# Kernel optimization log

Hardware: AMD Instinct MI355X
Metric: run time of the kernel (lower is better)

The kernel has to match this reference:

```python
import jax, jax.numpy as jnp
import numpy as np

B, N, M, D, H, K, V = 2, 2048, 2048, 1024, 16, 64, 64
MAX_WAVELENGTH = 10000
SCALE_FACTOR = 1.0


def rope(x, positions, max_wavelength, scale_factor):
    # x: [b, s, h, k]; positions: [b, s] int
    head_dim = x.shape[-1]
    fraction = 2.0 * jnp.arange(head_dim // 2, dtype=x.dtype) / head_dim
    timescale = jnp.asarray(max_wavelength, x.dtype) ** fraction            # [k/2]
    # scaled positions -> phase per (b, s, 1 head bcast, k/2)
    phase = (positions.astype(x.dtype) / scale_factor)[:, :, None, None] / timescale  # [b,s,1,k/2]
    sin, cos = jnp.sin(phase), jnp.cos(phase)
    x1, x2 = jnp.split(x, 2, axis=-1)
    return jnp.concatenate([x1 * cos - x2 * sin, x2 * cos + x1 * sin], axis=-1)


def setup_inputs() -> dict:
    key = jax.random.key(0)
    ks = jax.random.split(key, 8)
    scale = 1.0 / np.sqrt(D)  # keep logits numerically sane with random params
    inp = {
        "query": jax.random.normal(ks[0], (B, N, D), jnp.float32),
        "q_positions": jnp.broadcast_to(jnp.arange(N, dtype=jnp.int32), (B, N)),
        "key": jax.random.normal(ks[1], (B, M, D), jnp.float32),
        "k_positions": jnp.broadcast_to(jnp.arange(M, dtype=jnp.int32), (B, M)),
        "value": jax.random.normal(ks[2], (B, M, D), jnp.float32),
        "mask": jnp.ones((1, 1, N, M), dtype=bool),
        "P_q": jax.random.normal(ks[3], (H, D, K), jnp.float32) * scale,
        "P_k": jax.random.normal(ks[4], (H, D, K), jnp.float32) * scale,
        "P_v": jax.random.normal(ks[5], (H, D, V), jnp.float32) * scale,
        "P_o": jax.random.normal(ks[6], (H, D, V), jnp.float32) * scale,
    }
    return inp


def reference(query, q_positions, key, k_positions, value, mask, P_q, P_k, P_v, P_o):
    q = jnp.einsum('bnd,hdk->bnhk', query, P_q)
    k = jnp.einsum('bmd,hdk->bmhk', key, P_k)
    v = jnp.einsum('bmd,hdv->bmhv', value, P_v)
    q = rope(q, q_positions, MAX_WAVELENGTH, SCALE_FACTOR)
    k = rope(k, k_positions, MAX_WAVELENGTH, SCALE_FACTOR)
    logits = jnp.einsum('bnhk,bmhk->bhnm', q, k)
    if mask is not None:
        logits = jnp.where(mask, logits, -jnp.inf)
    weights = jax.nn.softmax(logits, axis=-1)
    o = jnp.einsum('bhnm,bmhv->bnhv', weights, v)
    return jnp.einsum('bnhv,hdv->bnd', o, P_o)
```

## Files before the change

kernel.cpp:

```cpp
#include <hip/hip_runtime.h>
#include <hip/hip_bf16.h>
#include <math.h>

#define B_ 2
#define N_ 2048
#define M_ 2048
#define D_ 1024
#define H_ 16


typedef _Float16 f16;
typedef f16  f16x4 __attribute__((ext_vector_type(4)));
typedef f16  f16x8 __attribute__((ext_vector_type(8)));
typedef float f32x4  __attribute__((ext_vector_type(4)));
typedef float f32x16 __attribute__((ext_vector_type(16)));

#define MFMA16(a, b, c) __builtin_amdgcn_mfma_f32_16x16x32_f16((a), (b), (c), 0, 0, 0)
#define MFMA32(a, b, c) __builtin_amdgcn_mfma_f32_32x32x16_f16((a), (b), (c), 0, 0, 0)
#define LDST 72

static __device__ __forceinline__ unsigned int pk2(float a, float b) {
  auto h = __builtin_amdgcn_cvt_pkrtz(a, b);
  return __builtin_bit_cast(unsigned int, h);
}

__global__ __launch_bounds__(256) void prep_all(
    const float* __restrict__ Pq, const float* __restrict__ Pk,
    const float* __restrict__ Pv, const float* __restrict__ Po,
    const int* __restrict__ qpos, const int* __restrict__ kpos,
    f16* __restrict__ Ptq, f16* __restrict__ Ptk, f16* __restrict__ Ptv,
    f16* __restrict__ Wo, float2* __restrict__ tabq, float2* __restrict__ tabk)
{
  __shared__ float Ts[64][65];
  const int z = blockIdx.y, x = blockIdx.x, tid = threadIdx.x;
  if (z < 3) {
    if (x >= 256) return;
    const float* P = (z == 0) ? Pq : (z == 1) ? Pk : Pv;
    f16* Pt = (z == 0) ? Ptq : (z == 1) ? Ptk : Ptv;
    const int d0 = (x & 15) * 64, h = x >> 4;
    #pragma unroll
    for (int it = 0; it < 4; ++it) {
      int fi = tid + 256 * it;
      int dr = fi >> 4, c4 = (fi & 15) << 2;
      float4 v = *(const float4*)(P + ((size_t)h * D_ + d0 + dr) * 64 + c4);
      Ts[dr][c4+0] = v.x; Ts[dr][c4+1] = v.y; Ts[dr][c4+2] = v.z; Ts[dr][c4+3] = v.w;
    }
    __syncthreads();
    const int c = tid >> 2, dp = (tid & 3) * 16;
    f16x8 w0, w1;
    #pragma unroll
    for (int i = 0; i < 8; ++i) { w0[i] = (f16)Ts[dp + i][c]; w1[i] = (f16)Ts[dp + 8 + i][c]; }
    f16* dst = Pt + ((size_t)h * 64 + c) * D_ + d0 + dp;
    *(f16x8*)dst = w0;
    *(f16x8*)(dst + 8) = w1;
  } else if (z == 3) {
    int e = (x * 256 + tid) * 4;
    if (e >= H_ * D_ * 64) return;
    int h = e >> 16, d = (e >> 6) & 1023, v = e & 63;
    float4 xx = *(const float4*)(Po + e);
    f16x4 w = {(f16)xx.x, (f16)xx.y, (f16)xx.z, (f16)xx.w};
    *(f16x4*)&Wo[(size_t)d * 1024 + h * 64 + v] = w;
  } else {
    if (x >= 512) return;
    int idx = x * 256 + tid;
    int r = idx >> 5, c = idx & 31;
    const int* pos = (z == 4) ? qpos : kpos;
    float2* tab = (z == 4) ? tabq : tabk;
    float fpos = (float)pos[r];
    float inv_ts = exp2f(-(float)c * 0.4152410118609203f);
    float ph = fpos * inv_ts, sn, cs;
    sincosf(ph, &sn, &cs);
    tab[idx] = make_float2(cs, sn);
  }
}

__global__ __launch_bounds__(256) void gemm_fused(
    const float* __restrict__ Aq, const float* __restrict__ Ak,
    const float* __restrict__ Av,
    const f16* __restrict__ Bq, const f16* __restrict__ Bk,
    const f16* __restrict__ Bv,
    const float2* __restrict__ tabq, const float2* __restrict__ tabk,
    f16* __restrict__ dq, f16* __restrict__ dk, f16* __restrict__ dv)
{
  __shared__ f16 As[128 * LDST];
  __shared__ f16 Bs[128 * LDST];
  const int tid = threadIdx.x, lane = tid & 63, wave = tid >> 6;
  const int quad = lane >> 4, l16 = lane & 15;
  const int col0 = blockIdx.x * 128, row0 = blockIdx.y * 128;
  const int op = blockIdx.z;
  const int wr = (wave >> 1) * 64, wc = (wave & 1) * 64;

  const float* A  = (op == 0) ? Aq : (op == 1) ? Ak : Av;
  const f16*  Bt  = (op == 0) ? Bq : (op == 1) ? Bk : Bv;

  f32x4 acc[4][4] = {};
  float4 apre[8];
  f16x8  bpre[4];

  #pragma unroll
  for (int it = 0; it < 8; ++it) {
    int fi = tid + 256 * it;
    int row = fi >> 4, c4 = (fi & 15) << 2;
    apre[it] = *(const float4*)(A + (size_t)(row0 + row) * 1024 + c4);
  }
  #pragma unroll
  for (int it = 0; it < 4; ++it) {
    int fi = tid + 256 * it;
    int row = fi >> 3, c8 = (fi & 7) * 8;
    bpre[it] = *(const f16x8*)(Bt + (size_t)(col0 + row) * 1024 + c8);
  }

  for (int k0 = 0; k0 < 1024; k0 += 64) {
    __syncthreads();
    #pragma unroll
    for (int it = 0; it < 8; ++it) {
      int fi = tid + 256 * it;
      int row = fi >> 4, c4 = (fi & 15) << 2;
      f16x4 hv = {(f16)apre[it].x, (f16)apre[it].y, (f16)apre[it].z, (f16)apre[it].w};
      *(f16x4*)&As[row * LDST + c4] = hv;
    }
    #pragma unroll
    for (int it = 0; it < 4; ++it) {
      int fi = tid + 256 * it;
      int row = fi >> 3, c8 = (fi & 7) * 8;
      *(f16x8*)&Bs[row * LDST + c8] = bpre[it];
    }
    __syncthreads();
    if (k0 + 64 < 1024) {
      #pragma unroll
      for (int it = 0; it < 8; ++it) {
        int fi = tid + 256 * it;
        int row = fi >> 4, c4 = (fi & 15) << 2;
        apre[it] = *(const float4*)(A + (size_t)(row0 + row) * 1024 + k0 + 64 + c4);
      }
      #pragma unroll
      for (int it = 0; it < 4; ++it) {
        int fi = tid + 256 * it;
        int row = fi >> 3, c8 = (fi & 7) * 8;
        bpre[it] = *(const f16x8*)(Bt + (size_t)(col0 + row) * 1024 + k0 + 64 + c8);
      }
    }
    #pragma unroll
    for (int ks = 0; ks < 2; ++ks) {
      f16x8 af[4], bf[4];
      #pragma unroll
      for (int i = 0; i < 4; ++i)
        af[i] = *(const f16x8*)&As[(wr + i * 16 + l16) * LDST + ks * 32 + quad * 8];
      #pragma unroll
      for (int j = 0; j < 4; ++j)
        bf[j] = *(const f16x8*)&Bs[(wc + j * 16 + l16) * LDST + ks * 32 + quad * 8];
      #pragma unroll
      for (int i = 0; i < 4; ++i)
        #pragma unroll
        for (int j = 0; j < 4; ++j)
          acc[i][j] = MFMA16(af[i], bf[j], acc[i][j]);
    }
  }

  if (op == 2) {
    #pragma unroll
    for (int i = 0; i < 4; ++i) {
      int r = row0 + wr + i * 16 + quad * 4;
      int b = r >> 11, s = r & 2047;
      #pragma unroll
      for (int j = 0; j < 4; ++j) {
        int col = col0 + wc + j * 16 + l16;
        int h = col >> 6, v = col & 63;
        f16x4 w = {(f16)acc[i][j][0], (f16)acc[i][j][1],
                   (f16)acc[i][j][2], (f16)acc[i][j][3]};
        *(f16x4*)&dv[((size_t)(b * H_ + h) * 64 + v) * 2048 + s] = w;
      }
    }
  } else {
    const float2* tab = (op == 0) ? tabq : tabk;
    f16* oq = (op == 0) ? dq : dk;
    #pragma unroll
    for (int i = 0; i < 4; ++i) {
      #pragma unroll
      for (int reg = 0; reg < 4; ++reg) {
        int r = row0 + wr + i * 16 + quad * 4 + reg;
        int b = r >> 11, s = r & 2047;
        #pragma unroll
        for (int j = 0; j < 2; ++j) {
          int col = col0 + wc + j * 16 + l16;
          int h = col >> 6, c = col & 63;
          float2 cs = tab[r * 32 + c];
          float x1 = acc[i][j][reg], x2 = acc[i][j + 2][reg];
          size_t base = ((size_t)(b * H_ + h) * 2048 + s) * 64;
          oq[base + c]      = (f16)(x1 * cs.x - x2 * cs.y);
          oq[base + c + 32] = (f16)(x2 * cs.x + x1 * cs.y);
        }
      }
    }
  }
}

__global__ __launch_bounds__(256, 2) void flash6(
    const f16* __restrict__ q, const f16* __restrict__ k,
    const f16* __restrict__ vt, f16* __restrict__ o)
{
  __shared__ f16 Ks[64 * LDST];
  __shared__ f16 Vts[64 * LDST];

  const int tid = threadIdx.x, lane = tid & 63, wave = tid >> 6;
  const int L = lane >> 5, nl = lane & 31;
  const int n0 = blockIdx.x * 128;
  const int h = blockIdx.y, b = blockIdx.z;

  const f16* qb = q  + (size_t)(b * H_ + h) * N_ * 64;
  const f16* kb = k  + (size_t)(b * H_ + h) * M_ * 64;
  const f16* vb = vt + (size_t)(b * H_ + h) * 64 * M_;

  f16x8 qf[4];
  #pragma unroll
  for (int g = 0; g < 4; ++g)
    qf[g] = *(const f16x8*)(qb + (size_t)(n0 + wave * 32 + nl) * 64 + g * 16 + L * 8);

  f32x16 acc[2] = {};
  float mst = -INFINITY;
  float lst = 0.f;
  const float L2E = 1.4426950408889634f;

  const int srow = tid >> 2, soff = (tid & 3) * 16;

  f16x8 kp0 = *(const f16x8*)(kb + (size_t)srow * 64 + soff);
  f16x8 kp1 = *(const f16x8*)(kb + (size_t)srow * 64 + soff + 8);
  f16x8 vp0 = *(const f16x8*)(vb + (size_t)srow * M_ + soff);
  f16x8 vp1 = *(const f16x8*)(vb + (size_t)srow * M_ + soff + 8);

  for (int m0 = 0; m0 < M_; m0 += 64) {
    __syncthreads();
    *(f16x8*)&Ks[srow * LDST + soff]      = kp0;
    *(f16x8*)&Ks[srow * LDST + soff + 8]  = kp1;
    *(f16x8*)&Vts[srow * LDST + soff]     = vp0;
    *(f16x8*)&Vts[srow * LDST + soff + 8] = vp1;
    __syncthreads();
    if (m0 + 64 < M_) {
      kp0 = *(const f16x8*)(kb + (size_t)(m0 + 64 + srow) * 64 + soff);
      kp1 = *(const f16x8*)(kb + (size_t)(m0 + 64 + srow) * 64 + soff + 8);
      vp0 = *(const f16x8*)(vb + (size_t)srow * M_ + m0 + 64 + soff);
      vp1 = *(const f16x8*)(vb + (size_t)srow * M_ + m0 + 64 + soff + 8);
    }

    f32x16 s[2] = {};
    __builtin_amdgcn_s_setprio(1);
    #pragma unroll
    for (int u = 0; u < 2; ++u)
      #pragma unroll
      for (int g = 0; g < 4; ++g) {
        f16x8 af = *(const f16x8*)&Ks[(u * 32 + nl) * LDST + g * 16 + L * 8];
        s[u] = MFMA32(af, qf[g], s[u]);
      }
    __builtin_amdgcn_s_setprio(0);

    float tm[16];
    #pragma unroll
    for (int r = 0; r < 16; ++r) tm[r] = fmaxf(s[0][r], s[1][r]);
    #pragma unroll
    for (int st = 8; st >= 1; st >>= 1)
      #pragma unroll
      for (int r = 0; r < st; ++r) tm[r] = fmaxf(tm[r], tm[r + st]);
    float mx = fmaxf(tm[0], __shfl_xor(tm[0], 32));
    float mx2 = mx * L2E;
    float m_new = fmaxf(mst, mx2);

    if (!__all(mx2 - mst <= 8.0f)) {
      float alpha = exp2f(mst - m_new);
      #pragma unroll
      for (int u = 0; u < 2; ++u)
        #pragma unroll
        for (int r = 0; r < 16; ++r) acc[u][r] *= alpha;
      lst *= alpha;
      mst = m_new;
    }

    float p[2][16];
    #pragma unroll
    for (int u = 0; u < 2; ++u)
      #pragma unroll
      for (int r = 0; r < 16; ++r)
        p[u][r] = exp2f(s[u][r] * L2E - mst);

    float ts[16];
    #pragma unroll
    for (int r = 0; r < 16; ++r) ts[r] = p[0][r] + p[1][r];
    #pragma unroll
    for (int st = 8; st >= 1; st >>= 1)
      #pragma unroll
      for (int r = 0; r < st; ++r) ts[r] += ts[r + st];
    float sum = ts[0];
    sum += __shfl_xor(sum, 32);
    lst += sum;

    unsigned int qw[2][4][2];
    #pragma unroll
    for (int u = 0; u < 2; ++u)
      #pragma unroll
      for (int rq = 0; rq < 4; ++rq) {
        qw[u][rq][0] = pk2(p[u][rq * 4 + 0], p[u][rq * 4 + 1]);
        qw[u][rq][1] = pk2(p[u][rq * 4 + 2], p[u][rq * 4 + 3]);
      }
    union PBu { unsigned int w[4]; f16x8 v; } pb[4];
    #pragma unroll
    for (int u = 0; u < 2; ++u)
      #pragma unroll
      for (int gg = 0; gg < 2; ++gg)
        #pragma unroll
        for (int w = 0; w < 2; ++w) {
          unsigned int a = qw[u][2 * gg][w], bb = qw[u][2 * gg + 1][w];
          asm volatile("v_permlane32_swap_b32 %0, %1" : "+v"(a), "+v"(bb));
          pb[2 * u + gg].w[w]     = a;
          pb[2 * u + gg].w[2 + w] = bb;
        }

    __builtin_amdgcn_s_setprio(1);
    #pragma unroll
    for (int u = 0; u < 2; ++u)
      #pragma unroll
      for (int g = 0; g < 4; ++g) {
        f16x8 vf = *(const f16x8*)&Vts[(u * 32 + nl) * LDST + g * 16 + L * 8];
        acc[u] = MFMA32(vf, pb[g].v, acc[u]);
      }
    __builtin_amdgcn_s_setprio(0);
  }

  float invl = 1.0f / lst;
  f16* ob = o + ((size_t)(b * N_ + n0 + wave * 32 + nl) * 1024) + h * 64;
  #pragma unroll
  for (int u = 0; u < 2; ++u)
    #pragma unroll
    for (int rq = 0; rq < 4; ++rq) {
      f16x4 w = {(f16)(acc[u][rq * 4 + 0] * invl), (f16)(acc[u][rq * 4 + 1] * invl),
                 (f16)(acc[u][rq * 4 + 2] * invl), (f16)(acc[u][rq * 4 + 3] * invl)};
      *(f16x4*)&ob[u * 32 + 8 * rq + 4 * L] = w;
    }
}

__global__ __launch_bounds__(256) void gemm_out(
    const f16* __restrict__ A, const f16* __restrict__ Bt,
    float* __restrict__ out)
{
  __shared__ f16 As[128 * LDST];
  __shared__ f16 Bs[64 * LDST];
  const int tid = threadIdx.x, lane = tid & 63, wave = tid >> 6;
  const int quad = lane >> 4, l16 = lane & 15;
  const int col0 = blockIdx.x * 64, row0 = blockIdx.y * 128;
  const int wr = (wave >> 1) * 64, wc = (wave & 1) * 32;

  f32x4 acc[4][2] = {};
  f16x8 apre[4], bpre[2];

  #pragma unroll
  for (int it = 0; it < 4; ++it) {
    int fi = tid + 256 * it;
    int row = fi >> 3, c8 = (fi & 7) * 8;
    apre[it] = *(const f16x8*)(A + (size_t)(row0 + row) * 1024 + c8);
  }
  #pragma unroll
  for (int it = 0; it < 2; ++it) {
    int fi = tid + 256 * it;
    int row = fi >> 3, c8 = (fi & 7) * 8;
    bpre[it] = *(const f16x8*)(Bt + (size_t)(col0 + row) * 1024 + c8);
  }

  for (int k0 = 0; k0 < 1024; k0 += 64) {
    __syncthreads();
    #pragma unroll
    for (int it = 0; it < 4; ++it) {
      int fi = tid + 256 * it;
      int row = fi >> 3, c8 = (fi & 7) * 8;
      *(f16x8*)&As[row * LDST + c8] = apre[it];
    }
    #pragma unroll
    for (int it = 0; it < 2; ++it) {
      int fi = tid + 256 * it;
      int row = fi >> 3, c8 = (fi & 7) * 8;
      *(f16x8*)&Bs[row * LDST + c8] = bpre[it];
    }
    __syncthreads();
    if (k0 + 64 < 1024) {
      #pragma unroll
      for (int it = 0; it < 4; ++it) {
        int fi = tid + 256 * it;
        int row = fi >> 3, c8 = (fi & 7) * 8;
        apre[it] = *(const f16x8*)(A + (size_t)(row0 + row) * 1024 + k0 + 64 + c8);
      }
      #pragma unroll
      for (int it = 0; it < 2; ++it) {
        int fi = tid + 256 * it;
        int row = fi >> 3, c8 = (fi & 7) * 8;
        bpre[it] = *(const f16x8*)(Bt + (size_t)(col0 + row) * 1024 + k0 + 64 + c8);
      }
    }
    #pragma unroll
    for (int ks = 0; ks < 2; ++ks) {
      f16x8 af[4], bf[2];
      #pragma unroll
      for (int i = 0; i < 4; ++i)
        af[i] = *(const f16x8*)&As[(wr + i * 16 + l16) * LDST + ks * 32 + quad * 8];
      #pragma unroll
      for (int j = 0; j < 2; ++j)
        bf[j] = *(const f16x8*)&Bs[(wc + j * 16 + l16) * LDST + ks * 32 + quad * 8];
      #pragma unroll
      for (int i = 0; i < 4; ++i)
        #pragma unroll
        for (int j = 0; j < 2; ++j)
          acc[i][j] = MFMA16(af[i], bf[j], acc[i][j]);
    }
  }

  #pragma unroll
  for (int i = 0; i < 4; ++i)
    #pragma unroll
    for (int j = 0; j < 2; ++j)
      #pragma unroll
      for (int reg = 0; reg < 4; ++reg)
        out[(size_t)(row0 + wr + i * 16 + quad * 4 + reg) * 1024 +
            col0 + wc + j * 16 + l16] = acc[i][j][reg];
}

extern "C" void kernel_launch(void* const* d_in, const int* in_sizes, int n_in,
                              void* d_out, int out_size, void* d_ws, size_t ws_size,
                              hipStream_t stream) {
  (void)in_sizes; (void)n_in; (void)out_size; (void)ws_size;
  const float* query = (const float*)d_in[0];
  const int*   qpos  = (const int*)d_in[1];
  const float* key   = (const float*)d_in[2];
  const int*   kpos  = (const int*)d_in[3];
  const float* value = (const float*)d_in[4];
  const float* Pq = (const float*)d_in[6];
  const float* Pk = (const float*)d_in[7];
  const float* Pv = (const float*)d_in[8];
  const float* Po = (const float*)d_in[9];
  float* out = (float*)d_out;

  const size_t pm = (size_t)1024 * 1024;
  const size_t em = (size_t)B_ * H_ * 2048 * 64;
  f16* Ptq = (f16*)d_ws;
  f16* Ptk = Ptq + pm;
  f16* Ptv = Ptk + pm;
  f16* Wo  = Ptv + pm;
  f16* q_ws  = Wo + pm;
  f16* k_ws  = q_ws + em;
  f16* vt_ws = k_ws + em;
  f16* o_ws  = vt_ws + em;
  float2* tabq = (float2*)(o_ws + em);
  float2* tabk = tabq + (size_t)4096 * 32;

  dim3 blk(256);
  prep_all<<<dim3(1024, 6), blk, 0, stream>>>(
      Pq, Pk, Pv, Po, qpos, kpos, Ptq, Ptk, Ptv, Wo, tabq, tabk);

  gemm_fused<<<dim3(8, 32, 3), blk, 0, stream>>>(
      query, key, value, Ptq, Ptk, Ptv, tabq, tabk, q_ws, k_ws, vt_ws);

  flash6<<<dim3(N_ / 128, H_, B_), blk, 0, stream>>>(q_ws, k_ws, vt_ws, o_ws);

  gemm_out<<<dim3(16, 32), blk, 0, stream>>>(o_ws, Wo, out);
}
```

Baseline: 265.7 us.

## Split flash attention KV range across two wave groups and merge partials

The flash kernel now runs 512 threads per block, with two groups of four waves each covering half of the key/value sequence for the same 128 query rows. After the loop, group 1 writes its partial accumulators plus running max and sum to shared memory, and group 0 combines them with log-sum-exp rescaling before writing the output. The aim is more waves per CU and a shorter serial KV loop, since the grid of 512 blocks was small. The cost is an extra merge step, more shared memory, and a 512-thread block with launch bounds that may limit registers per thread.

```diff
diff --git a/kernel.cpp b/kernel.cpp
--- a/kernel.cpp
+++ b/kernel.cpp
@@ -195,47 +195,51 @@
   }
 }
 
-__global__ __launch_bounds__(256, 2) void flash6(
+__global__ __launch_bounds__(512, 4) void flash7(
     const f16* __restrict__ q, const f16* __restrict__ k,
     const f16* __restrict__ vt, f16* __restrict__ o)
 {
-  __shared__ f16 Ks[64 * LDST];
-  __shared__ f16 Vts[64 * LDST];
+  __shared__ __align__(16) char smem[4 * 64 * LDST * sizeof(f16)];
 
   const int tid = threadIdx.x, lane = tid & 63, wave = tid >> 6;
+  const int g = wave >> 2, w4 = wave & 3;
   const int L = lane >> 5, nl = lane & 31;
   const int n0 = blockIdx.x * 128;
   const int h = blockIdx.y, b = blockIdx.z;
 
+  f16* Ks  = (f16*)smem + (size_t)g * (64 * LDST);
+  f16* Vts = (f16*)smem + (size_t)(2 + g) * (64 * LDST);
+
   const f16* qb = q  + (size_t)(b * H_ + h) * N_ * 64;
-  const f16* kb = k  + (size_t)(b * H_ + h) * M_ * 64;
-  const f16* vb = vt + (size_t)(b * H_ + h) * 64 * M_;
+  const f16* kb = k  + (size_t)(b * H_ + h) * M_ * 64 + (size_t)g * 1024 * 64;
+  const f16* vb = vt + (size_t)(b * H_ + h) * 64 * M_ + g * 1024;
 
   f16x8 qf[4];
   #pragma unroll
-  for (int g = 0; g < 4; ++g)
-    qf[g] = *(const f16x8*)(qb + (size_t)(n0 + wave * 32 + nl) * 64 + g * 16 + L * 8);
+  for (int gg = 0; gg < 4; ++gg)
+    qf[gg] = *(const f16x8*)(qb + (size_t)(n0 + w4 * 32 + nl) * 64 + gg * 16 + L * 8);
 
   f32x16 acc[2] = {};
   float mst = -INFINITY;
   float lst = 0.f;
   const float L2E = 1.4426950408889634f;
 
-  const int srow = tid >> 2, soff = (tid & 3) * 16;
+  const int gtid = tid & 255;
+  const int srow = gtid >> 2, soff = (gtid & 3) * 16;
 
   f16x8 kp0 = *(const f16x8*)(kb + (size_t)srow * 64 + soff);
   f16x8 kp1 = *(const f16x8*)(kb + (size_t)srow * 64 + soff + 8);
   f16x8 vp0 = *(const f16x8*)(vb + (size_t)srow * M_ + soff);
   f16x8 vp1 = *(const f16x8*)(vb + (size_t)srow * M_ + soff + 8);
 
-  for (int m0 = 0; m0 < M_; m0 += 64) {
+  for (int m0 = 0; m0 < 1024; m0 += 64) {
     __syncthreads();
     *(f16x8*)&Ks[srow * LDST + soff]      = kp0;
     *(f16x8*)&Ks[srow * LDST + soff + 8]  = kp1;
     *(f16x8*)&Vts[srow * LDST + soff]     = vp0;
     *(f16x8*)&Vts[srow * LDST + soff + 8] = vp1;
     __syncthreads();
-    if (m0 + 64 < M_) {
+    if (m0 + 64 < 1024) {
       kp0 = *(const f16x8*)(kb + (size_t)(m0 + 64 + srow) * 64 + soff);
       kp1 = *(const f16x8*)(kb + (size_t)(m0 + 64 + srow) * 64 + soff + 8);
       vp0 = *(const f16x8*)(vb + (size_t)srow * M_ + m0 + 64 + soff);
@@ -247,9 +251,9 @@
     #pragma unroll
     for (int u = 0; u < 2; ++u)
       #pragma unroll
-      for (int g = 0; g < 4; ++g) {
-        f16x8 af = *(const f16x8*)&Ks[(u * 32 + nl) * LDST + g * 16 + L * 8];
-        s[u] = MFMA32(af, qf[g], s[u]);
+      for (int gg = 0; gg < 4; ++gg) {
+        f16x8 af = *(const f16x8*)&Ks[(u * 32 + nl) * LDST + gg * 16 + L * 8];
+        s[u] = MFMA32(af, qf[gg], s[u]);
       }
     __builtin_amdgcn_s_setprio(0);
 
@@ -317,23 +321,40 @@
     #pragma unroll
     for (int u = 0; u < 2; ++u)
       #pragma unroll
-      for (int g = 0; g < 4; ++g) {
-        f16x8 vf = *(const f16x8*)&Vts[(u * 32 + nl) * LDST + g * 16 + L * 8];
-        acc[u] = MFMA32(vf, pb[g].v, acc[u]);
+      for (int gg = 0; gg < 4; ++gg) {
+        f16x8 vf = *(const f16x8*)&Vts[(u * 32 + nl) * LDST + gg * 16 + L * 8];
+        acc[u] = MFMA32(vf, pb[gg].v, acc[u]);
       }
     __builtin_amdgcn_s_setprio(0);
   }
 
-  float invl = 1.0f / lst;
-  f16* ob = o + ((size_t)(b * N_ + n0 + wave * 32 + nl) * 1024) + h * 64;
-  #pragma unroll
-  for (int u = 0; u < 2; ++u)
-    #pragma unroll
-    for (int rq = 0; rq < 4; ++rq) {
-      f16x4 w = {(f16)(acc[u][rq * 4 + 0] * invl), (f16)(acc[u][rq * 4 + 1] * invl),
-                 (f16)(acc[u][rq * 4 + 2] * invl), (f16)(acc[u][rq * 4 + 3] * invl)};
-      *(f16x4*)&ob[u * 32 + 8 * rq + 4 * L] = w;
-    }
+  float* mrg = (float*)smem;
+  const int mb = (w4 * 64 + lane) * 34;
+  __syncthreads();
+  if (g == 1) {
+    #pragma unroll
+    for (int r = 0; r < 16; ++r) { mrg[mb + r] = acc[0][r]; mrg[mb + 16 + r] = acc[1][r]; }
+    mrg[mb + 32] = mst;
+    mrg[mb + 33] = lst;
+  }
+  __syncthreads();
+  if (g == 0) {
+    float m1 = mrg[mb + 32], l1 = mrg[mb + 33];
+    float Mm = fmaxf(mst, m1);
+    float a0 = exp2f(mst - Mm), a1 = exp2f(m1 - Mm);
+    float invl = 1.0f / (a0 * lst + a1 * l1);
+    f16* ob = o + ((size_t)(b * N_ + n0 + w4 * 32 + nl) * 1024) + h * 64;
+    #pragma unroll
+    for (int u = 0; u < 2; ++u)
+      #pragma unroll
+      for (int rq = 0; rq < 4; ++rq) {
+        f16x4 w;
+        #pragma unroll
+        for (int j = 0; j < 4; ++j)
+          w[j] = (f16)((a0 * acc[u][rq * 4 + j] + a1 * mrg[mb + u * 16 + rq * 4 + j]) * invl);
+        *(f16x4*)&ob[u * 32 + 8 * rq + 4 * L] = w;
+      }
+  }
 }
 
 __global__ __launch_bounds__(256) void gemm_out(
@@ -454,7 +475,7 @@
   gemm_fused<<<dim3(8, 32, 3), blk, 0, stream>>>(
       query, key, value, Ptq, Ptk, Ptv, tabq, tabk, q_ws, k_ws, vt_ws);
 
-  flash6<<<dim3(N_ / 128, H_, B_), blk, 0, stream>>>(q_ws, k_ws, vt_ws, o_ws);
+  flash7<<<dim3(N_ / 128, H_, B_), dim3(512), 0, stream>>>(q_ws, k_ws, vt_ws, o_ws);
 
   gemm_out<<<dim3(16, 32), blk, 0, stream>>>(o_ws, Wo, out);
 }
```

Result: no change. 262.9 us (-1.0%).
